# Optimization experiments

Measured on AMD Instinct MI355X. Metric: run time of the kernel, lower is better.

## Reference

```python
import jax, jax.numpy as jnp
import numpy as np

N_NODES = 100000
N_EDGES = 800000
IN_F, H_F, OUT_F = 512, 256, 64
N_EXPERTS = 4  # k = 1


def _normalize_edges(edge_index, n):
    """gcn_norm: add self loops, symmetric D^-1/2 A D^-1/2 edge weights."""
    loop = jnp.arange(n, dtype=edge_index.dtype)
    row = jnp.concatenate([edge_index[0], loop])
    col = jnp.concatenate([edge_index[1], loop])
    w = jnp.ones(row.shape[0], dtype=jnp.float32)
    deg = jax.ops.segment_sum(w, col, num_segments=n)  # in-degree incl. self loop
    dinv = jnp.where(deg > 0, deg ** -0.5, 0.0)
    norm = dinv[row] * w * dinv[col]
    return row, col, norm


def _propagate(x, row, col, norm, n):
    # message x_j * edge_weight, scatter-add at destination col
    msgs = x[row] * norm[:, None]
    return jax.ops.segment_sum(msgs, col, num_segments=n)


def _moe_linear(x, w_gate, expert_w, expert_b):
    # eval-mode noisy top-k gating with k=1: clean logits, top-1, softmax over
    # a single logit -> gate value 1.0 for the selected expert.
    logits = x @ w_gate                         # [N, E]
    idx = jnp.argmax(logits, axis=-1)           # [N]
    gates = jax.nn.one_hot(idx, N_EXPERTS, dtype=x.dtype)  # [N, E]
    y_all = jnp.einsum('ni,eio->neo', x, expert_w) + expert_b[None]  # [N, E, H]
    return jnp.einsum('ne,neo->no', gates, y_all)


def setup_inputs() -> dict:
    key = jax.random.key(0)
    ks = jax.random.split(key, 8)
    x = jax.random.normal(ks[0], (N_NODES, IN_F), dtype=jnp.float32)
    edge_index = jax.random.randint(ks[1], (2, N_EDGES), 0, N_NODES, dtype=jnp.int64)
    w_gate = jax.random.normal(ks[2], (IN_F, N_EXPERTS), dtype=jnp.float32) * 0.05
    expert_w = jax.random.normal(ks[3], (N_EXPERTS, IN_F, H_F), dtype=jnp.float32) * (1.0 / np.sqrt(IN_F))
    expert_b = jnp.zeros((N_EXPERTS, H_F), dtype=jnp.float32)
    bias1 = jnp.zeros((H_F,), dtype=jnp.float32)
    w2 = jax.random.normal(ks[4], (H_F, OUT_F), dtype=jnp.float32) * (1.0 / np.sqrt(H_F))
    bias2 = jnp.zeros((OUT_F,), dtype=jnp.float32)
    return {"x": x, "edge_index": edge_index, "w_gate": w_gate,
            "expert_w": expert_w, "expert_b": expert_b, "bias1": bias1,
            "w2": w2, "bias2": bias2}


def reference(x, edge_index, w_gate, expert_w, expert_b, bias1, w2, bias2):
    n = x.shape[0]
    row, col, norm = _normalize_edges(edge_index, n)
    # conv1: MoE linear -> propagate -> bias
    h = _moe_linear(x, w_gate, expert_w, expert_b)
    h = _propagate(h, row, col, norm, n) + bias1
    h = jax.nn.relu(h)
    # dropout is identity at eval
    # conv2: plain GCNConv
    h = h @ w2
    h = _propagate(h, row, col, norm, n) + bias2
    return jax.nn.log_softmax(h, axis=1)
```

## Files before the change

kernel.cpp:

```cpp
#include <hip/hip_runtime.h>
#include <math.h>

typedef __bf16 bf16x8 __attribute__((ext_vector_type(8)));
typedef float f32x16 __attribute__((ext_vector_type(16)));
typedef float f32x4v __attribute__((ext_vector_type(4)));

__device__ __forceinline__ unsigned short f2bf(float f) {
  union { float f; unsigned int u; } v; v.f = f;
  unsigned int r = (v.u + 0x7FFFu + ((v.u >> 16) & 1u)) >> 16;
  return (unsigned short)r;
}
__device__ __forceinline__ float bf2f(unsigned short u) {
  union { unsigned int u; float f; } v; v.u = ((unsigned int)u) << 16;
  return v.f;
}
__device__ __forceinline__ void bf2x(unsigned int u, float& lo, float& hi) {
  union { unsigned int u; float f; } a, b;
  a.u = u << 16; b.u = u & 0xFFFF0000u;
  lo = a.f; hi = b.f;
}
__device__ __forceinline__ void gload16(const void* g, void* l) {
  __builtin_amdgcn_global_load_lds(
      (__attribute__((address_space(1))) void*)const_cast<void*>(g),
      (__attribute__((address_space(3))) void*)l, 16, 0, 0);
}

__global__ void k_init(int* cnt, int* meta, int N) {
  int i = blockIdx.x * blockDim.x + threadIdx.x;
  if (i < N) cnt[i] = 0;
  if (i < 32) meta[i] = 0;
}

__global__ __launch_bounds__(256) void k_scanA(const int* __restrict__ cnt,
                                               int* __restrict__ incl,
                                               int* __restrict__ bsums, int N,
                                               const int* __restrict__ eidx,
                                               int* __restrict__ meta,
                                               int* __restrict__ perm, int nb) {
  int tid = threadIdx.x;
  if (blockIdx.x >= (unsigned)nb) {
    __shared__ int lhist[4];
    __shared__ int lbase[4];
    if (tid < 4) lhist[tid] = 0;
    __syncthreads();
    int n = (blockIdx.x - nb) * 256 + tid;
    int e = 0, lrank = 0;
    bool valid = (n < N);
    if (valid) {
      e = eidx[n];
      lrank = atomicAdd(&lhist[e], 1);
    }
    __syncthreads();
    if (tid < 4) {
      int c = lhist[tid];
      int eo = 0;
      #pragma unroll
      for (int k = 0; k < 4; ++k) if (k < tid) eo += meta[k];
      lbase[tid] = eo + ((c > 0) ? atomicAdd(&meta[18 + tid], c) : 0);
    }
    __syncthreads();
    if (valid) perm[lbase[e] + lrank] = n;
    return;
  }
  __shared__ int s[1024];
  int base = blockIdx.x * 1024;
  #pragma unroll
  for (int t = 0; t < 4; ++t) {
    int i = tid + t * 256;
    int idx = base + i;
    s[i] = (idx < N) ? cnt[idx] : 0;
  }
  __syncthreads();
  for (int d = 1; d < 1024; d <<= 1) {
    int v[4];
    #pragma unroll
    for (int t = 0; t < 4; ++t) {
      int i = tid + t * 256;
      v[t] = (i >= d) ? s[i - d] : 0;
    }
    __syncthreads();
    #pragma unroll
    for (int t = 0; t < 4; ++t) {
      int i = tid + t * 256;
      s[i] += v[t];
    }
    __syncthreads();
  }
  #pragma unroll
  for (int t = 0; t < 4; ++t) {
    int i = tid + t * 256;
    int idx = base + i;
    if (idx < N) incl[idx] = s[i];
  }
  if (tid == 0) bsums[blockIdx.x] = s[1023];
}

__global__ __launch_bounds__(256) void k_scanC(const int* __restrict__ cnt,
                                               const int* __restrict__ incl,
                                               const int* __restrict__ bsums,
                                               int* __restrict__ rowptr,
                                               int* __restrict__ cursor,
                                               float* __restrict__ dinv,
                                               int* __restrict__ meta, int N, int E) {
  __shared__ int sboff;
  int idx1024 = blockIdx.x >> 2;
  if (threadIdx.x < 64) {
    int s = 0;
    for (int k = threadIdx.x; k < idx1024; k += 64) s += bsums[k];
    #pragma unroll
    for (int off = 32; off > 0; off >>= 1) s += __shfl_xor(s, off, 64);
    if (threadIdx.x == 0) sboff = s;
  }
  __syncthreads();
  int i = blockIdx.x * blockDim.x + threadIdx.x;
  if (i < N) {
    int ex = incl[i] - cnt[i] + sboff;
    rowptr[i] = ex;
    cursor[i] = ex;
    dinv[i] = rsqrtf((float)(cnt[i] + 1));
    if (i == 0) rowptr[N] = E;
  }
  if (blockIdx.x == 0 && threadIdx.x == 0) {
    int* hist = meta;
    int* eoff = meta + 4;
    int* toff = meta + 9;
    int* ecur = meta + 14;
    int s = 0, t = 0;
    eoff[0] = 0; toff[0] = 0;
    for (int e = 0; e < 4; ++e) {
      s += hist[e];
      eoff[e + 1] = s;
      t += (hist[e] + 127) / 128;
      toff[e + 1] = t;
      ecur[e] = eoff[e];
    }
  }
}

__global__ void k_scatter(const int* __restrict__ row, const int* __restrict__ col,
                          int* __restrict__ cursor, const float* __restrict__ dinv,
                          int2* __restrict__ csr2, int E) {
  int e = blockIdx.x * blockDim.x + threadIdx.x;
  if (e < E) {
    int c = col[e];
    int r = row[e];
    int p = atomicAdd(&cursor[c], 1);
    csr2[p] = make_int2(r, __float_as_int(dinv[r]));
  }
}

__global__ __launch_bounds__(256) void k_gate(const float* __restrict__ x,
                                              const float* __restrict__ wg,
                                              int* __restrict__ eidx,
                                              int* __restrict__ meta,
                                              unsigned short* __restrict__ xb,
                                              const int* __restrict__ col,
                                              int* __restrict__ cnt,
                                              const float* __restrict__ ew,
                                              unsigned short* __restrict__ ewb,
                                              const float* __restrict__ w2,
                                              unsigned short* __restrict__ w2b,
                                              int N, int E, int gateB, int cntB) {
  int tid = threadIdx.x;
  int b = blockIdx.x;
  int usedC = min(cntB, gateB / 2);
  int mix3 = 3 * usedC;
  int role, idx;
  if (b < mix3) {
    if ((b % 3) == 2) { role = 1; idx = b / 3; }
    else              { role = 0; idx = (b / 3) * 2 + (b % 3); }
  } else {
    int r = b - mix3;
    int gLeft = gateB - 2 * usedC;
    if (r < gLeft) { role = 0; idx = 2 * usedC + r; }
    else {
      r -= gLeft;
      int cLeft = cntB - usedC;
      if (r < cLeft) { role = 1; idx = usedC + r; }
      else           { role = 2; idx = r - cLeft; }
    }
  }

  if (role == 1) {
    int e = idx * 256 + tid;
    if (e < E) atomicAdd(&cnt[col[e]], 1);
    return;
  }
  if (role == 2) {
    if (idx < 256) {
      int n = tid;
      int eidx2 = idx >> 6, kc = idx & 63;
      const float* src = ew + ((size_t)eidx2 * 512 + (size_t)kc * 8) * 256 + n;
      unsigned short tmp[8];
      #pragma unroll
      for (int ke = 0; ke < 8; ++ke) tmp[ke] = f2bf(src[(size_t)ke * 256]);
      *(uint4*)(ewb + ((size_t)idx * 256 + n) * 8) = *(const uint4*)tmp;
    } else {
      int kc = idx - 256;
      if (tid < 64) {
        const float* src = w2 + (size_t)kc * 8 * 64 + tid;
        unsigned short tmp[8];
        #pragma unroll
        for (int ke = 0; ke < 8; ++ke) tmp[ke] = f2bf(src[(size_t)ke * 64]);
        *(uint4*)(w2b + ((size_t)kc * 64 + tid) * 8) = *(const uint4*)tmp;
      }
    }
    return;
  }

  __shared__ float wgT[4][512];
  __shared__ int lhist[4];
  if (tid < 4) lhist[tid] = 0;
  {
    int r0 = tid * 2;
    float4 wa = *(const float4*)(wg + 4 * r0);
    float4 wb = *(const float4*)(wg + 4 * (r0 + 1));
    wgT[0][r0] = wa.x; wgT[1][r0] = wa.y; wgT[2][r0] = wa.z; wgT[3][r0] = wa.w;
    wgT[0][r0 + 1] = wb.x; wgT[1][r0 + 1] = wb.y; wgT[2][r0 + 1] = wb.z; wgT[3][r0 + 1] = wb.w;
  }
  __syncthreads();
  int node = idx * 16 + (tid >> 4);
  int sl = tid & 15;
  if (node < N) {
    const float* xr = x + (size_t)node * 512;
    unsigned short* xbr = xb + (size_t)node * 512;
    f32x4v xv[8];
    #pragma unroll
    for (int j = 0; j < 8; ++j) {
      asm volatile("global_load_dwordx4 %0, %1, off"
                   : "=v"(xv[j])
                   : "v"(xr + 4 * (sl + 16 * j)));
    }
    asm volatile("s_waitcnt vmcnt(0)");
    __builtin_amdgcn_sched_barrier(0);
    #pragma unroll
    for (int j = 0; j < 8; ++j) {
      ushort4 ov;
      ov.x = f2bf(xv[j].x); ov.y = f2bf(xv[j].y); ov.z = f2bf(xv[j].z); ov.w = f2bf(xv[j].w);
      *(ushort4*)(xbr + 4 * (sl + 16 * j)) = ov;
    }
    float l0 = 0.f, l1 = 0.f, l2 = 0.f, l3 = 0.f;
    #pragma unroll
    for (int j = 0; j < 8; ++j) {
      int k0 = 4 * (sl + 16 * j);
      float4 w0 = *(const float4*)&wgT[0][k0];
      float4 w1 = *(const float4*)&wgT[1][k0];
      float4 w2v = *(const float4*)&wgT[2][k0];
      float4 w3 = *(const float4*)&wgT[3][k0];
      l0 += xv[j].x * w0.x + xv[j].y * w0.y + xv[j].z * w0.z + xv[j].w * w0.w;
      l1 += xv[j].x * w1.x + xv[j].y * w1.y + xv[j].z * w1.z + xv[j].w * w1.w;
      l2 += xv[j].x * w2v.x + xv[j].y * w2v.y + xv[j].z * w2v.z + xv[j].w * w2v.w;
      l3 += xv[j].x * w3.x + xv[j].y * w3.y + xv[j].z * w3.z + xv[j].w * w3.w;
    }
    #pragma unroll
    for (int off = 8; off > 0; off >>= 1) {
      l0 += __shfl_xor(l0, off, 64);
      l1 += __shfl_xor(l1, off, 64);
      l2 += __shfl_xor(l2, off, 64);
      l3 += __shfl_xor(l3, off, 64);
    }
    if (sl == 0) {
      int a = 0; float best = l0;
      if (l1 > best) { best = l1; a = 1; }
      if (l2 > best) { best = l2; a = 2; }
      if (l3 > best) { best = l3; a = 3; }
      eidx[node] = a;
      atomicAdd(&lhist[a], 1);
    }
  }
  __syncthreads();
  if (tid < 4 && lhist[tid] > 0) atomicAdd(&meta[tid], lhist[tid]);
}

__global__ __launch_bounds__(512, 2) void k_gemm1(const unsigned short* __restrict__ xb,
                                                  const unsigned short* __restrict__ ewb,
                                                  const float* __restrict__ eb,
                                                  const int* __restrict__ perm,
                                                  const int* __restrict__ meta,
                                                  unsigned short* __restrict__ h1) {
  __shared__ __align__(16) unsigned short A_lds[8192];
  __shared__ __align__(16) unsigned short B_lds[16384];
  __shared__ int sperm[128];
  const int* eoff = meta + 4;
  const int* toff = meta + 9;
  int v = blockIdx.x;
  if (v >= toff[4]) return;
  int e = 0;
  while (v >= toff[e + 1]) ++e;
  int m0 = eoff[e] + (v - toff[e]) * 128;
  int mEnd = eoff[e + 1];
  int tid = threadIdx.x;

  if (tid < 128) {
    int m = m0 + tid;
    sperm[tid] = perm[(m < mEnd) ? m : (mEnd - 1)];
  }
  __syncthreads();

  int wave = tid >> 6, lane = tid & 63;
  int wr = wave >> 2, wc = wave & 3;
  int hi = lane >> 5, lo = lane & 31;
  int r128 = tid & 127;

  f32x16 acc[2][2];
  #pragma unroll
  for (int mi = 0; mi < 2; ++mi)
    #pragma unroll
    for (int ni = 0; ni < 2; ++ni)
      #pragma unroll
      for (int r = 0; r < 16; ++r) acc[mi][ni][r] = 0.f;

  const unsigned short* arow = xb + (size_t)sperm[r128] * 512;
  int kclA = tid >> 7;
  const uint4* ebase = (const uint4*)(ewb + (size_t)e * 64 * 2048);

  for (int k0 = 0; k0 < 512; k0 += 64) {
    __syncthreads();
    gload16(arow + k0 + kclA * 8,       &A_lds[((size_t)kclA * 128 + r128) * 8]);
    gload16(arow + k0 + (kclA + 4) * 8, &A_lds[((size_t)(kclA + 4) * 128 + r128) * 8]);
    const uint4* bsrc = ebase + (size_t)(k0 >> 3) * 256;
    gload16(bsrc + tid,        &B_lds[((size_t)0 * 512 + tid) * 8]);
    gload16(bsrc + 512 + tid,  &B_lds[((size_t)1 * 512 + tid) * 8]);
    gload16(bsrc + 1024 + tid, &B_lds[((size_t)2 * 512 + tid) * 8]);
    gload16(bsrc + 1536 + tid, &B_lds[((size_t)3 * 512 + tid) * 8]);
    __syncthreads();
    #pragma unroll
    for (int s = 0; s < 4; ++s) {
      int kcl = s * 2 + hi;
      bf16x8 a0f = *(const bf16x8*)&A_lds[((size_t)kcl * 128 + wr * 64 + lo) * 8];
      bf16x8 a1f = *(const bf16x8*)&A_lds[((size_t)kcl * 128 + wr * 64 + 32 + lo) * 8];
      bf16x8 b0f = *(const bf16x8*)&B_lds[((size_t)kcl * 256 + wc * 64 + lo) * 8];
      bf16x8 b1f = *(const bf16x8*)&B_lds[((size_t)kcl * 256 + wc * 64 + 32 + lo) * 8];
      acc[0][0] = __builtin_amdgcn_mfma_f32_32x32x16_bf16(a0f, b0f, acc[0][0], 0, 0, 0);
      acc[0][1] = __builtin_amdgcn_mfma_f32_32x32x16_bf16(a0f, b1f, acc[0][1], 0, 0, 0);
      acc[1][0] = __builtin_amdgcn_mfma_f32_32x32x16_bf16(a1f, b0f, acc[1][0], 0, 0, 0);
      acc[1][1] = __builtin_amdgcn_mfma_f32_32x32x16_bf16(a1f, b1f, acc[1][1], 0, 0, 0);
    }
  }

  #pragma unroll
  for (int ni = 0; ni < 2; ++ni) {
    int col = wc * 64 + ni * 32 + lo;
    float bias = eb[e * 256 + col];
    #pragma unroll
    for (int mi = 0; mi < 2; ++mi) {
      #pragma unroll
      for (int q = 0; q < 4; ++q) {
        #pragma unroll
        for (int j = 0; j < 4; ++j) {
          int r = j + 8 * q + 4 * hi;
          int lrow = wr * 64 + mi * 32 + r;
          if (m0 + lrow < mEnd) {
            h1[(size_t)sperm[lrow] * 256 + col] = f2bf(acc[mi][ni][q * 4 + j] + bias);
          }
        }
      }
    }
  }
}

__global__ __launch_bounds__(256) void k_prop1(const unsigned short* __restrict__ h1,
                                               const int* __restrict__ rowptr,
                                               const int2* __restrict__ csr2,
                                               const float* __restrict__ dinv,
                                               const float* __restrict__ bias1,
                                               unsigned short* __restrict__ hrelu, int N) {
  int tid = threadIdx.x;
  int c = blockIdx.x * 8 + (tid >> 5);
  int l = tid & 31;
  if (c >= N) return;
  float dc = dinv[c];
  const uint4* hr = (const uint4*)h1;
  uint4 sv = hr[(size_t)c * 32 + l];
  float slf = dc * dc;
  float a0, a1, a2, a3, a4, a5, a6, a7;
  {
    float lo, hi;
    bf2x(sv.x, lo, hi); a0 = lo * slf; a1 = hi * slf;
    bf2x(sv.y, lo, hi); a2 = lo * slf; a3 = hi * slf;
    bf2x(sv.z, lo, hi); a4 = lo * slf; a5 = hi * slf;
    bf2x(sv.w, lo, hi); a6 = lo * slf; a7 = hi * slf;
  }
  int jb = rowptr[c], je = rowptr[c + 1];
  int j = jb;
  #define ACC8(v, s) { float lo, hi; \
    bf2x((v).x, lo, hi); a0 += lo * (s); a1 += hi * (s); \
    bf2x((v).y, lo, hi); a2 += lo * (s); a3 += hi * (s); \
    bf2x((v).z, lo, hi); a4 += lo * (s); a5 += hi * (s); \
    bf2x((v).w, lo, hi); a6 += lo * (s); a7 += hi * (s); }
  for (; j + 7 < je; j += 8) {
    int2 rc[8];
    #pragma unroll
    for (int t = 0; t < 8; ++t) rc[t] = csr2[j + t];
    uint4 vv[8];
    #pragma unroll
    for (int t = 0; t < 8; ++t) vv[t] = hr[(size_t)rc[t].x * 32 + l];
    #pragma unroll
    for (int t = 0; t < 8; ++t) {
      float s = __int_as_float(rc[t].y) * dc;
      ACC8(vv[t], s);
    }
  }
  for (; j + 3 < je; j += 4) {
    int2 rc0 = csr2[j], rc1 = csr2[j + 1], rc2 = csr2[j + 2], rc3 = csr2[j + 3];
    uint4 v0 = hr[(size_t)rc0.x * 32 + l];
    uint4 v1 = hr[(size_t)rc1.x * 32 + l];
    uint4 v2 = hr[(size_t)rc2.x * 32 + l];
    uint4 v3 = hr[(size_t)rc3.x * 32 + l];
    float s0 = __int_as_float(rc0.y) * dc, s1 = __int_as_float(rc1.y) * dc;
    float s2 = __int_as_float(rc2.y) * dc, s3 = __int_as_float(rc3.y) * dc;
    ACC8(v0, s0); ACC8(v1, s1); ACC8(v2, s2); ACC8(v3, s3);
  }
  for (; j < je; ++j) {
    int2 rc = csr2[j];
    float s = __int_as_float(rc.y) * dc;
    uint4 v = hr[(size_t)rc.x * 32 + l];
    ACC8(v, s);
  }
  #undef ACC8
  float4 b01 = *(const float4*)(bias1 + l * 8);
  float4 b23 = *(const float4*)(bias1 + l * 8 + 4);
  a0 = fmaxf(a0 + b01.x, 0.f); a1 = fmaxf(a1 + b01.y, 0.f);
  a2 = fmaxf(a2 + b01.z, 0.f); a3 = fmaxf(a3 + b01.w, 0.f);
  a4 = fmaxf(a4 + b23.x, 0.f); a5 = fmaxf(a5 + b23.y, 0.f);
  a6 = fmaxf(a6 + b23.z, 0.f); a7 = fmaxf(a7 + b23.w, 0.f);
  uint4 ov;
  ov.x = ((unsigned int)f2bf(a1) << 16) | f2bf(a0);
  ov.y = ((unsigned int)f2bf(a3) << 16) | f2bf(a2);
  ov.z = ((unsigned int)f2bf(a5) << 16) | f2bf(a4);
  ov.w = ((unsigned int)f2bf(a7) << 16) | f2bf(a6);
  ((uint4*)hrelu)[(size_t)c * 32 + l] = ov;
}

__global__ __launch_bounds__(256, 2) void k_gemm2(const unsigned short* __restrict__ A,
                                                  const unsigned short* __restrict__ w2b,
                                                  unsigned short* __restrict__ h3, int N) {
  __shared__ __align__(16) unsigned short B_lds[16384];
  __shared__ __align__(16) unsigned short A_lds[8192];
  int tid = threadIdx.x;
  int m0 = blockIdx.x * 128;
  #pragma unroll
  for (int it = 0; it < 8; ++it)
    gload16(((const uint4*)w2b) + it * 256 + tid, &B_lds[((size_t)it * 256 + tid) * 8]);

  int wave = tid >> 6, lane = tid & 63;
  int wr = wave >> 1, wc = wave & 1;
  int hi = lane >> 5, lo = lane & 31;

  f32x16 acc[2];
  #pragma unroll
  for (int mi = 0; mi < 2; ++mi)
    #pragma unroll
    for (int r = 0; r < 16; ++r) acc[mi][r] = 0.f;

  int i = tid & 127;
  int row = m0 + i;
  if (row >= N) row = N - 1;
  const unsigned short* arow = A + (size_t)row * 256;
  int kcl0 = tid >> 7;

  for (int k0 = 0; k0 < 256; k0 += 64) {
    __syncthreads();
    #pragma unroll
    for (int t = 0; t < 4; ++t)
      gload16(arow + k0 + (kcl0 + 2 * t) * 8,
              &A_lds[((size_t)(kcl0 + 2 * t) * 128 + i) * 8]);
    __syncthreads();
    #pragma unroll
    for (int s = 0; s < 4; ++s) {
      int kcl = s * 2 + hi;
      bf16x8 a0f = *(const bf16x8*)&A_lds[((size_t)kcl * 128 + wr * 64 + lo) * 8];
      bf16x8 a1f = *(const bf16x8*)&A_lds[((size_t)kcl * 128 + wr * 64 + 32 + lo) * 8];
      bf16x8 bf = *(const bf16x8*)&B_lds[(((size_t)(k0 >> 3) + kcl) * 64 + wc * 32 + lo) * 8];
      acc[0] = __builtin_amdgcn_mfma_f32_32x32x16_bf16(a0f, bf, acc[0], 0, 0, 0);
      acc[1] = __builtin_amdgcn_mfma_f32_32x32x16_bf16(a1f, bf, acc[1], 0, 0, 0);
    }
  }

  int n = wc * 32 + lo;
  #pragma unroll
  for (int mi = 0; mi < 2; ++mi) {
    #pragma unroll
    for (int q = 0; q < 4; ++q) {
      #pragma unroll
      for (int j = 0; j < 4; ++j) {
        int r = j + 8 * q + 4 * hi;
        int orow = m0 + wr * 64 + mi * 32 + r;
        if (orow < N) h3[(size_t)orow * 64 + n] = f2bf(acc[mi][q * 4 + j]);
      }
    }
  }
}

__global__ __launch_bounds__(256) void k_prop2(const unsigned short* __restrict__ h3,
                                               const int* __restrict__ rowptr,
                                               const int2* __restrict__ csr2,
                                               const float* __restrict__ dinv,
                                               const float* __restrict__ bias2,
                                               float* __restrict__ out, int N) {
  int tid = threadIdx.x;
  int c = blockIdx.x * 32 + (tid >> 3);
  int l = tid & 7;
  if (c >= N) return;
  float dc = dinv[c];
  const uint4* hr = (const uint4*)h3;
  uint4 sv = hr[(size_t)c * 8 + l];
  float slf = dc * dc;
  float a0, a1, a2, a3, a4, a5, a6, a7;
  {
    float lo, hi;
    bf2x(sv.x, lo, hi); a0 = lo * slf; a1 = hi * slf;
    bf2x(sv.y, lo, hi); a2 = lo * slf; a3 = hi * slf;
    bf2x(sv.z, lo, hi); a4 = lo * slf; a5 = hi * slf;
    bf2x(sv.w, lo, hi); a6 = lo * slf; a7 = hi * slf;
  }
  int jb = rowptr[c], je = rowptr[c + 1];
  int j = jb;
  #define ACC8(v, s) { float lo, hi; \
    bf2x((v).x, lo, hi); a0 += lo * (s); a1 += hi * (s); \
    bf2x((v).y, lo, hi); a2 += lo * (s); a3 += hi * (s); \
    bf2x((v).z, lo, hi); a4 += lo * (s); a5 += hi * (s); \
    bf2x((v).w, lo, hi); a6 += lo * (s); a7 += hi * (s); }
  for (; j + 7 < je; j += 8) {
    int2 rc[8];
    #pragma unroll
    for (int t = 0; t < 8; ++t) rc[t] = csr2[j + t];
    uint4 vv[8];
    #pragma unroll
    for (int t = 0; t < 8; ++t) vv[t] = hr[(size_t)rc[t].x * 8 + l];
    #pragma unroll
    for (int t = 0; t < 8; ++t) {
      float s = __int_as_float(rc[t].y) * dc;
      ACC8(vv[t], s);
    }
  }
  for (; j + 3 < je; j += 4) {
    int2 rc0 = csr2[j], rc1 = csr2[j + 1], rc2 = csr2[j + 2], rc3 = csr2[j + 3];
    uint4 v0 = hr[(size_t)rc0.x * 8 + l];
    uint4 v1 = hr[(size_t)rc1.x * 8 + l];
    uint4 v2 = hr[(size_t)rc2.x * 8 + l];
    uint4 v3 = hr[(size_t)rc3.x * 8 + l];
    float s0 = __int_as_float(rc0.y) * dc, s1 = __int_as_float(rc1.y) * dc;
    float s2 = __int_as_float(rc2.y) * dc, s3 = __int_as_float(rc3.y) * dc;
    ACC8(v0, s0); ACC8(v1, s1); ACC8(v2, s2); ACC8(v3, s3);
  }
  for (; j < je; ++j) {
    int2 rc = csr2[j];
    float s = __int_as_float(rc.y) * dc;
    uint4 v = hr[(size_t)rc.x * 8 + l];
    ACC8(v, s);
  }
  #undef ACC8
  float4 b01 = *(const float4*)(bias2 + l * 8);
  float4 b23 = *(const float4*)(bias2 + l * 8 + 4);
  a0 += b01.x; a1 += b01.y; a2 += b01.z; a3 += b01.w;
  a4 += b23.x; a5 += b23.y; a6 += b23.z; a7 += b23.w;
  float m = fmaxf(fmaxf(fmaxf(a0, a1), fmaxf(a2, a3)), fmaxf(fmaxf(a4, a5), fmaxf(a6, a7)));
  #pragma unroll
  for (int off = 4; off > 0; off >>= 1) m = fmaxf(m, __shfl_xor(m, off, 64));
  float s = expf(a0 - m) + expf(a1 - m) + expf(a2 - m) + expf(a3 - m)
          + expf(a4 - m) + expf(a5 - m) + expf(a6 - m) + expf(a7 - m);
  #pragma unroll
  for (int off = 4; off > 0; off >>= 1) s += __shfl_xor(s, off, 64);
  float ls = m + logf(s);
  float* orow = out + (size_t)c * 64 + l * 8;
  float4 o0 = make_float4(a0 - ls, a1 - ls, a2 - ls, a3 - ls);
  float4 o1 = make_float4(a4 - ls, a5 - ls, a6 - ls, a7 - ls);
  *(float4*)orow = o0;
  *(float4*)(orow + 4) = o1;
}

extern "C" void kernel_launch(void* const* d_in, const int* in_sizes, int n_in,
                              void* d_out, int out_size, void* d_ws, size_t ws_size,
                              hipStream_t stream) {
  const float* x  = (const float*)d_in[0];
  const int*   ei = (const int*)d_in[1];
  const float* wg = (const float*)d_in[2];
  const float* ew = (const float*)d_in[3];
  const float* eb = (const float*)d_in[4];
  const float* b1 = (const float*)d_in[5];
  const float* w2 = (const float*)d_in[6];
  const float* b2 = (const float*)d_in[7];
  float* out = (float*)d_out;

  int N = in_sizes[0] / 512;
  int E = in_sizes[1] / 2;
  const int* row = ei;
  const int* col = ei + E;

  char* p = (char*)d_ws;
  auto alloc = [&](size_t bytes) -> void* {
    void* r = (void*)p;
    p += (bytes + 255) & ~(size_t)255;
    return r;
  };
  int*   cnt    = (int*)alloc((size_t)N * 4);
  int*   rowptr = (int*)alloc((size_t)(N + 1) * 4);
  int*   cursor = (int*)alloc((size_t)N * 4);
  int*   bsums  = (int*)alloc(1024 * 4);
  float* dinv   = (float*)alloc((size_t)N * 4);
  int*   eidx   = (int*)alloc((size_t)N * 4);
  int*   meta   = (int*)alloc(32 * 4);
  int*   perm   = (int*)alloc((size_t)N * 4);
  int2*  csr2   = (int2*)alloc((size_t)E * 8);
  unsigned short* h1    = (unsigned short*)alloc((size_t)N * 256 * 2);
  unsigned short* hrelu = (unsigned short*)alloc((size_t)N * 256 * 2);
  unsigned short* h3    = (unsigned short*)alloc((size_t)N * 64 * 2);
  unsigned short* xb  = (unsigned short*)alloc((size_t)N * 512 * 2);
  unsigned short* ewb = (unsigned short*)alloc((size_t)4 * 512 * 256 * 2);
  unsigned short* w2b = (unsigned short*)alloc((size_t)256 * 64 * 2);

  int nb = (N + 1023) / 1024;
  int gateB = (N + 15) / 16;
  int cntB = (E + 255) / 256;
  int scatB = (E + 255) / 256;
  int binB = (N + 255) / 256;

  k_init<<<(N + 255) / 256, 256, 0, stream>>>(cnt, meta, N);
  k_gate<<<gateB + cntB + 288, 256, 0, stream>>>(x, wg, eidx, meta, xb, col, cnt,
                                                 ew, ewb, w2, w2b, N, E, gateB, cntB);
  k_scanA<<<nb + binB, 256, 0, stream>>>(cnt, rowptr, bsums, N, eidx, meta, perm, nb);
  k_scanC<<<(N + 255) / 256, 256, 0, stream>>>(cnt, rowptr, bsums, rowptr, cursor, dinv,
                                               meta, N, E);
  k_scatter<<<scatB, 256, 0, stream>>>(row, col, cursor, dinv, csr2, E);
  int ntiles = (N + 127) / 128 + 4;
  k_gemm1<<<ntiles, 512, 0, stream>>>(xb, ewb, eb, perm, meta, h1);
  k_prop1<<<(N + 7) / 8, 256, 0, stream>>>(h1, rowptr, csr2, dinv, b1, hrelu, N);
  k_gemm2<<<(N + 127) / 128, 256, 0, stream>>>(hrelu, w2b, h3, N);
  k_prop2<<<(N + 31) / 32, 256, 0, stream>>>(h3, rowptr, csr2, dinv, b2, out, N);
}
```

Measured before the change: 347.8 us.

## Convert x to bf16 inside GEMM1 and fuse edge scatter into GEMM1 launch

Removes the bf16 copy of x written by the gate kernel; GEMM1 now loads fp32 rows of x directly, converts them in registers and stores them to LDS. This removes a 100MB write and 100MB read of the xb intermediate. The edge-scatter kernel is also folded into the GEMM1 launch as extra blocks, which saves one launch and lets the scatter overlap with the GEMM. In exchange, GEMM1 reads twice as many bytes for A and replaces async LDS loads with synchronous register loads before the barrier, which may expose more latency.

Measured after the change: 348.4 us. No clear change (+0.2%).

```diff
diff --git a/kernel.cpp b/kernel.cpp
--- a/kernel.cpp
+++ b/kernel.cpp
@@ -137,23 +137,10 @@
   }
 }
 
-__global__ void k_scatter(const int* __restrict__ row, const int* __restrict__ col,
-                          int* __restrict__ cursor, const float* __restrict__ dinv,
-                          int2* __restrict__ csr2, int E) {
-  int e = blockIdx.x * blockDim.x + threadIdx.x;
-  if (e < E) {
-    int c = col[e];
-    int r = row[e];
-    int p = atomicAdd(&cursor[c], 1);
-    csr2[p] = make_int2(r, __float_as_int(dinv[r]));
-  }
-}
-
 __global__ __launch_bounds__(256) void k_gate(const float* __restrict__ x,
                                               const float* __restrict__ wg,
                                               int* __restrict__ eidx,
                                               int* __restrict__ meta,
-                                              unsigned short* __restrict__ xb,
                                               const int* __restrict__ col,
                                               int* __restrict__ cnt,
                                               const float* __restrict__ ew,
@@ -223,7 +210,6 @@
   int sl = tid & 15;
   if (node < N) {
     const float* xr = x + (size_t)node * 512;
-    unsigned short* xbr = xb + (size_t)node * 512;
     f32x4v xv[8];
     #pragma unroll
     for (int j = 0; j < 8; ++j) {
@@ -233,12 +219,6 @@
     }
     asm volatile("s_waitcnt vmcnt(0)");
     __builtin_amdgcn_sched_barrier(0);
-    #pragma unroll
-    for (int j = 0; j < 8; ++j) {
-      ushort4 ov;
-      ov.x = f2bf(xv[j].x); ov.y = f2bf(xv[j].y); ov.z = f2bf(xv[j].z); ov.w = f2bf(xv[j].w);
-      *(ushort4*)(xbr + 4 * (sl + 16 * j)) = ov;
-    }
     float l0 = 0.f, l1 = 0.f, l2 = 0.f, l3 = 0.f;
     #pragma unroll
     for (int j = 0; j < 8; ++j) {
@@ -272,12 +252,28 @@
   if (tid < 4 && lhist[tid] > 0) atomicAdd(&meta[tid], lhist[tid]);
 }
 
-__global__ __launch_bounds__(512, 2) void k_gemm1(const unsigned short* __restrict__ xb,
+__global__ __launch_bounds__(512, 2) void k_gemm1(const float* __restrict__ x,
                                                   const unsigned short* __restrict__ ewb,
                                                   const float* __restrict__ eb,
                                                   const int* __restrict__ perm,
                                                   const int* __restrict__ meta,
-                                                  unsigned short* __restrict__ h1) {
+                                                  unsigned short* __restrict__ h1,
+                                                  const int* __restrict__ erow,
+                                                  const int* __restrict__ ecol,
+                                                  int* __restrict__ cursor,
+                                                  const float* __restrict__ dinv,
+                                                  int2* __restrict__ csr2, int E, int gemmB) {
+  int tid = threadIdx.x;
+  if (blockIdx.x >= (unsigned)gemmB) {
+    int e = (blockIdx.x - gemmB) * 512 + tid;
+    if (e < E) {
+      int c = ecol[e];
+      int r = erow[e];
+      int p = atomicAdd(&cursor[c], 1);
+      csr2[p] = make_int2(r, __float_as_int(dinv[r]));
+    }
+    return;
+  }
   __shared__ __align__(16) unsigned short A_lds[8192];
   __shared__ __align__(16) unsigned short B_lds[16384];
   __shared__ int sperm[128];
@@ -289,7 +285,6 @@
   while (v >= toff[e + 1]) ++e;
   int m0 = eoff[e] + (v - toff[e]) * 128;
   int mEnd = eoff[e + 1];
-  int tid = threadIdx.x;
 
   if (tid < 128) {
     int m = m0 + tid;
@@ -301,6 +296,7 @@
   int wr = wave >> 2, wc = wave & 3;
   int hi = lane >> 5, lo = lane & 31;
   int r128 = tid & 127;
+  int q = tid >> 7;
 
   f32x16 acc[2][2];
   #pragma unroll
@@ -310,19 +306,30 @@
       #pragma unroll
       for (int r = 0; r < 16; ++r) acc[mi][ni][r] = 0.f;
 
-  const unsigned short* arow = xb + (size_t)sperm[r128] * 512;
-  int kclA = tid >> 7;
+  const float* axrow = x + (size_t)sperm[r128] * 512;
   const uint4* ebase = (const uint4*)(ewb + (size_t)e * 64 * 2048);
 
   for (int k0 = 0; k0 < 512; k0 += 64) {
-    __syncthreads();
-    gload16(arow + k0 + kclA * 8,       &A_lds[((size_t)kclA * 128 + r128) * 8]);
-    gload16(arow + k0 + (kclA + 4) * 8, &A_lds[((size_t)(kclA + 4) * 128 + r128) * 8]);
+    float4 af[4];
+    #pragma unroll
+    for (int t = 0; t < 4; ++t)
+      af[t] = *(const float4*)(axrow + k0 + q * 16 + t * 4);
+    __syncthreads();
     const uint4* bsrc = ebase + (size_t)(k0 >> 3) * 256;
     gload16(bsrc + tid,        &B_lds[((size_t)0 * 512 + tid) * 8]);
     gload16(bsrc + 512 + tid,  &B_lds[((size_t)1 * 512 + tid) * 8]);
     gload16(bsrc + 1024 + tid, &B_lds[((size_t)2 * 512 + tid) * 8]);
     gload16(bsrc + 1536 + tid, &B_lds[((size_t)3 * 512 + tid) * 8]);
+    unsigned short tmp[16];
+    #pragma unroll
+    for (int t = 0; t < 4; ++t) {
+      tmp[t * 4 + 0] = f2bf(af[t].x);
+      tmp[t * 4 + 1] = f2bf(af[t].y);
+      tmp[t * 4 + 2] = f2bf(af[t].z);
+      tmp[t * 4 + 3] = f2bf(af[t].w);
+    }
+    *(uint4*)&A_lds[((size_t)(q * 2 + 0) * 128 + r128) * 8] = *(const uint4*)&tmp[0];
+    *(uint4*)&A_lds[((size_t)(q * 2 + 1) * 128 + r128) * 8] = *(const uint4*)&tmp[8];
     __syncthreads();
     #pragma unroll
     for (int s = 0; s < 4; ++s) {
@@ -345,13 +352,13 @@
     #pragma unroll
     for (int mi = 0; mi < 2; ++mi) {
       #pragma unroll
-      for (int q = 0; q < 4; ++q) {
+      for (int qq = 0; qq < 4; ++qq) {
         #pragma unroll
         for (int j = 0; j < 4; ++j) {
-          int r = j + 8 * q + 4 * hi;
+          int r = j + 8 * qq + 4 * hi;
           int lrow = wr * 64 + mi * 32 + r;
           if (m0 + lrow < mEnd) {
-            h1[(size_t)sperm[lrow] * 256 + col] = f2bf(acc[mi][ni][q * 4 + j] + bias);
+            h1[(size_t)sperm[lrow] * 256 + col] = f2bf(acc[mi][ni][qq * 4 + j] + bias);
           }
         }
       }
@@ -606,25 +613,24 @@
   unsigned short* h1    = (unsigned short*)alloc((size_t)N * 256 * 2);
   unsigned short* hrelu = (unsigned short*)alloc((size_t)N * 256 * 2);
   unsigned short* h3    = (unsigned short*)alloc((size_t)N * 64 * 2);
-  unsigned short* xb  = (unsigned short*)alloc((size_t)N * 512 * 2);
   unsigned short* ewb = (unsigned short*)alloc((size_t)4 * 512 * 256 * 2);
   unsigned short* w2b = (unsigned short*)alloc((size_t)256 * 64 * 2);
 
   int nb = (N + 1023) / 1024;
   int gateB = (N + 15) / 16;
   int cntB = (E + 255) / 256;
-  int scatB = (E + 255) / 256;
   int binB = (N + 255) / 256;
+  int scatB512 = (E + 511) / 512;
 
   k_init<<<(N + 255) / 256, 256, 0, stream>>>(cnt, meta, N);
-  k_gate<<<gateB + cntB + 288, 256, 0, stream>>>(x, wg, eidx, meta, xb, col, cnt,
+  k_gate<<<gateB + cntB + 288, 256, 0, stream>>>(x, wg, eidx, meta, col, cnt,
                                                  ew, ewb, w2, w2b, N, E, gateB, cntB);
   k_scanA<<<nb + binB, 256, 0, stream>>>(cnt, rowptr, bsums, N, eidx, meta, perm, nb);
   k_scanC<<<(N + 255) / 256, 256, 0, stream>>>(cnt, rowptr, bsums, rowptr, cursor, dinv,
                                                meta, N, E);
-  k_scatter<<<scatB, 256, 0, stream>>>(row, col, cursor, dinv, csr2, E);
   int ntiles = (N + 127) / 128 + 4;
-  k_gemm1<<<ntiles, 512, 0, stream>>>(xb, ewb, eb, perm, meta, h1);
+  k_gemm1<<<ntiles + scatB512, 512, 0, stream>>>(x, ewb, eb, perm, meta, h1,
+                                                 row, col, cursor, dinv, csr2, E, ntiles);
   k_prop1<<<(N + 7) / 8, 256, 0, stream>>>(h1, rowptr, csr2, dinv, b1, hrelu, N);
   k_gemm2<<<(N + 127) / 128, 256, 0, stream>>>(hrelu, w2b, h3, N);
   k_prop2<<<(N + 31) / 32, 256, 0, stream>>>(h3, rowptr, csr2, dinv, b2, out, N);
```
